# Performance work log

Measured on AMD Instinct MI355X. Metric: run time of the kernel, lower is better.

The kernel has to match this reference:

```python
import jax, jax.numpy as jnp
import numpy as np

B, N, NODE_DIM = 256, 200, 2
H, D, L, FF = 8, 128, 3, 512
KD = D // H  # key/val dim per head = 16
EPS = 1e-5


def _uniform(key, shape, fan):
    s = 1.0 / np.sqrt(fan)
    return jax.random.uniform(key, shape, jnp.float32, -s, s)


def setup_inputs() -> dict:
    key = jax.random.key(0)
    ks = jax.random.split(key, 16)
    return {
        "x": jax.random.normal(ks[0], (B, N, NODE_DIM), jnp.float32),
        "Wemb": _uniform(ks[1], (NODE_DIM, D), NODE_DIM),
        "bemb": _uniform(ks[2], (D,), NODE_DIM),
        "Wq": _uniform(ks[3], (L, H, D, KD), KD),
        "Wk": _uniform(ks[4], (L, H, D, KD), KD),
        "Wv": _uniform(ks[5], (L, H, D, KD), KD),
        "Wo": _uniform(ks[6], (L, H, KD, D), D),
        "bn1_g": jnp.ones((L, D), jnp.float32),
        "bn1_b": jnp.zeros((L, D), jnp.float32),
        "W1": _uniform(ks[7], (L, D, FF), D),
        "b1": _uniform(ks[8], (L, FF), D),
        "W2": _uniform(ks[9], (L, FF, D), FF),
        "b2": _uniform(ks[10], (L, D), FF),
        "bn2_g": jnp.ones((L, D), jnp.float32),
        "bn2_b": jnp.zeros((L, D), jnp.float32),
    }


def _batch_norm(h, g, b):
    # BatchNorm1d in training mode: stats over all (batch*graph) positions per channel
    hf = h.reshape(-1, h.shape[-1])
    m = hf.mean(axis=0)
    v = hf.var(axis=0)  # biased variance, as torch uses for normalization
    return (h - m) * jax.lax.rsqrt(v + EPS) * g + b


def _mha(h, Wq, Wk, Wv, Wo):
    # h: [B,N,D]; Wq/Wk/Wv: [H,D,KD]; Wo: [H,KD,D]
    Q = jnp.einsum('bnd,hdk->hbnk', h, Wq)
    K = jnp.einsum('bnd,hdk->hbnk', h, Wk)
    V = jnp.einsum('bnd,hdk->hbnk', h, Wv)
    scores = jnp.einsum('hbqk,hbnk->hbqn', Q, K) * (1.0 / np.sqrt(KD))
    attn = jax.nn.softmax(scores, axis=-1)
    heads = jnp.einsum('hbqn,hbnk->hbqk', attn, V)
    return jnp.einsum('hbqk,hkd->bqd', heads, Wo)


def reference(x, Wemb, bemb, Wq, Wk, Wv, Wo, bn1_g, bn1_b, W1, b1, W2, b2, bn2_g, bn2_b):
    h = x @ Wemb + bemb  # init_embed: [B,N,D]
    for l in range(L):
        h = h + _mha(h, Wq[l], Wk[l], Wv[l], Wo[l])
        h = _batch_norm(h, bn1_g[l], bn1_b[l])
        ff = jax.nn.relu(h @ W1[l] + b1[l]) @ W2[l] + b2[l]
        h = _batch_norm(h + ff, bn2_g[l], bn2_b[l])
    return (h, h.mean(axis=1))
```

## Files before the change

### kernel.cpp

```cpp
#include <hip/hip_runtime.h>
#include <math.h>

#define B_ 256
#define N_ 200
#define D_ 128
#define H_ 8
#define KD_ 16
#define L_ 3
#define FF_ 512
#define ROWS (B_*N_)
#define BND (ROWS*D_)

typedef float f32x4 __attribute__((ext_vector_type(4)));
typedef _Float16 f16x4 __attribute__((ext_vector_type(4)));
typedef _Float16 f16x8 __attribute__((ext_vector_type(8)));

__device__ __forceinline__ ushort f2h_bits(float f) {
  _Float16 h = (_Float16)f;
  union { _Float16 h; ushort u; } v; v.h = h; return v.u;
}
__device__ __forceinline__ void splith(float f, ushort& hi, ushort& lo) {
  _Float16 h = (_Float16)f;
  float hf = (float)h;
  _Float16 l = (_Float16)(f - hf);
  union { _Float16 h; ushort u; } a, b; a.h = h; b.h = l;
  hi = a.u; lo = b.u;
}

__global__ __launch_bounds__(256) void embed_kernel(const float* __restrict__ x,
    const float* __restrict__ Wemb, const float* __restrict__ bemb,
    float* __restrict__ hp, ushort* __restrict__ hhi, ushort* __restrict__ hlo)
{
  int i4 = blockIdx.x * 256 + threadIdx.x;
  int r  = i4 >> 5, c4 = i4 & 31;
  float x0 = x[2*r], x1 = x[2*r + 1];
  const float4 w0 = ((const float4*)Wemb)[c4];
  const float4 w1 = ((const float4*)Wemb)[32 + c4];
  const float4 bb = ((const float4*)bemb)[c4];
  float o[4];
  o[0] = fmaf(x0, w0.x, fmaf(x1, w1.x, bb.x));
  o[1] = fmaf(x0, w0.y, fmaf(x1, w1.y, bb.y));
  o[2] = fmaf(x0, w0.z, fmaf(x1, w1.z, bb.z));
  o[3] = fmaf(x0, w0.w, fmaf(x1, w1.w, bb.w));
  float4 of = { o[0], o[1], o[2], o[3] };
  ((float4*)hp)[i4] = of;
  ushort hi[4], lo[4];
#pragma unroll
  for (int k = 0; k < 4; k++) splith(o[k], hi[k], lo[k]);
  uint2 ph, pl;
  ph.x = (uint)hi[0] | ((uint)hi[1] << 16);
  ph.y = (uint)hi[2] | ((uint)hi[3] << 16);
  pl.x = (uint)lo[0] | ((uint)lo[1] << 16);
  pl.y = (uint)lo[2] | ((uint)lo[3] << 16);
  ((uint2*)hhi)[i4] = ph;
  ((uint2*)hlo)[i4] = pl;
}

__global__ __launch_bounds__(256) void t_wo(const float* __restrict__ Wo,
    ushort* __restrict__ dh)
{
  int i = blockIdx.x * 256 + threadIdx.x;
  int l = i / 16384, r = i % 16384;
  int n = r >> 7, k = r & 127;
  int hh = k >> 4, kd = k & 15;
  float w = Wo[l*16384 + hh*2048 + kd*128 + n];
  dh[i] = f2h_bits(w);
}
__global__ __launch_bounds__(256) void t_w2(const float* __restrict__ W2,
    ushort* __restrict__ dh)
{
  int i = blockIdx.x * 256 + threadIdx.x;
  int l = i / 65536, r = i % 65536;
  int d = r >> 9, f = r & 511;
  float w = W2[l*65536 + f*128 + d];
  dh[i] = f2h_bits(w);
}

__global__ __launch_bounds__(128) void init_scales(float* __restrict__ sc, float* __restrict__ sh)
{
  int c = threadIdx.x;
  sc[c] = 1.f;
  sh[c] = 0.f;
}

__global__ __launch_bounds__(128) void fold_qkv(const float* __restrict__ Wq,
    const float* __restrict__ Wk, const float* __restrict__ Wv,
    const float* __restrict__ sc, const float* __restrict__ sh,
    ushort* __restrict__ wh, float* __restrict__ bout)
{
  __shared__ float wsum[2];
  int n = blockIdx.x;
  int k = threadIdx.x;
  int which = n >> 7, hh = (n >> 4) & 7, kd = n & 15;
  const float* src = (which == 0) ? Wq : (which == 1) ? Wk : Wv;
  float w = src[hh*2048 + k*16 + kd];
  if (which == 0) w *= 0.25f * 1.44269504088896340736f;
  wh[n*128 + k] = f2h_bits(w * sc[k]);
  float p = sh[k] * w;
#pragma unroll
  for (int d = 1; d < 64; d <<= 1) p += __shfl_xor(p, d);
  if ((k & 63) == 0) wsum[k >> 6] = p;
  __syncthreads();
  if (k == 0) bout[n] = wsum[0] + wsum[1];
}

__global__ __launch_bounds__(128) void fold_w1(const float* __restrict__ W1,
    const float* __restrict__ b1, const float* __restrict__ sc, const float* __restrict__ sh,
    ushort* __restrict__ wh, float* __restrict__ bout)
{
  __shared__ float wsum[2];
  int f = blockIdx.x;
  int k = threadIdx.x;
  float w = W1[k*512 + f];
  wh[f*128 + k] = f2h_bits(w * sc[k]);
  float p = sh[k] * w;
#pragma unroll
  for (int d = 1; d < 64; d <<= 1) p += __shfl_xor(p, d);
  if ((k & 63) == 0) wsum[k >> 6] = p;
  __syncthreads();
  if (k == 0) bout[f] = b1[f] + wsum[0] + wsum[1];
}

template<int K, bool ALO, bool BIAS, bool RELU, bool RESIDBN,
         bool OUTQKV, bool OUT16, bool OUTHL, bool OUTF32, bool STATS>
__global__ __launch_bounds__(256, 2) void gemm_mfma(
    const ushort* __restrict__ Ahi, const ushort* __restrict__ Alo,
    const ushort* __restrict__ Wh,
    const float* __restrict__ bias,
    const float* __restrict__ residf, const float* __restrict__ rsc, const float* __restrict__ rsh,
    float* __restrict__ Cf, ushort* __restrict__ C16,
    ushort* __restrict__ Chl_hi, ushort* __restrict__ Chl_lo,
    float* __restrict__ psum, float* __restrict__ psq, int Ntot)
{
  __shared__ ushort AhiS[128*64];
  __shared__ ushort AloS[ALO ? 128*64 : 8];
  __shared__ ushort BhS [128*64];
  const int t    = threadIdx.x;
  const int bm   = blockIdx.y * 128;
  const int bn   = blockIdx.x * 128;
  const int lane = t & 63;
  const int w    = t >> 6, wm = w >> 1, wn = w & 1;
  const int quad = lane >> 4, l15 = lane & 15;

  f32x4 acc[4][4];
#pragma unroll
  for (int i = 0; i < 4; i++)
#pragma unroll
    for (int j = 0; j < 4; j++) acc[i][j] = (f32x4){0.f, 0.f, 0.f, 0.f};

  const ushort* AhiB = Ahi + (size_t)bm * K;
  const ushort* AloB = ALO ? (Alo + (size_t)bm * K) : nullptr;
  const ushort* BhB  = Wh  + (size_t)bn * K;

  for (int k0 = 0; k0 < K; k0 += 64) {
#pragma unroll
    for (int i = 0; i < 4; i++) {
      int idx = i * 256 + t;
      int row = idx >> 3, c = idx & 7;
      int k8  = c ^ (row & 7);
      size_t off = (size_t)row * K + k0 + k8 * 8;
      ((uint4*)AhiS)[idx] = *(const uint4*)(AhiB + off);
      if (ALO) ((uint4*)AloS)[idx] = *(const uint4*)(AloB + off);
      ((uint4*)BhS)[idx]  = *(const uint4*)(BhB + off);
    }
    __syncthreads();
#pragma unroll
    for (int ks = 0; ks < 2; ks++) {
      f16x8 ah[4], al[4], bh[4];
#pragma unroll
      for (int i = 0; i < 4; i++) {
        int row = wm * 64 + i * 16 + l15;
        int k8  = ks * 4 + quad;
        int ci  = k8 ^ (row & 7);
        ah[i] = ((const f16x8*)AhiS)[row * 8 + ci];
        if (ALO) al[i] = ((const f16x8*)AloS)[row * 8 + ci];
        int nrow = wn * 64 + i * 16 + l15;
        int cj   = k8 ^ (nrow & 7);
        bh[i] = ((const f16x8*)BhS)[nrow * 8 + cj];
      }
#pragma unroll
      for (int i = 0; i < 4; i++)
#pragma unroll
        for (int j = 0; j < 4; j++) {
          if (ALO) acc[i][j] = __builtin_amdgcn_mfma_f32_16x16x32_f16(al[i], bh[j], acc[i][j], 0, 0, 0);
          acc[i][j] = __builtin_amdgcn_mfma_f32_16x16x32_f16(ah[i], bh[j], acc[i][j], 0, 0, 0);
        }
    }
    __syncthreads();
  }

  float bv[4], scv[4], shv[4];
#pragma unroll
  for (int j = 0; j < 4; j++) {
    int col = bn + wn*64 + j*16 + l15;
    if (BIAS)    bv[j]  = bias[col];
    if (RESIDBN) { scv[j] = rsc[col]; shv[j] = rsh[col]; }
  }
  float sj[4] = {0.f,0.f,0.f,0.f}, qj[4] = {0.f,0.f,0.f,0.f};
#pragma unroll
  for (int i = 0; i < 4; i++) {
#pragma unroll
    for (int r = 0; r < 4; r++) {
      int row = bm + wm*64 + i*16 + quad*4 + r;
#pragma unroll
      for (int j = 0; j < 4; j++) {
        int col = bn + wn*64 + j*16 + l15;
        float v = acc[i][j][r];
        if (BIAS)    v += bv[j];
        if (RELU)    v = fmaxf(v, 0.f);
        if (RESIDBN) v += fmaf(residf[(size_t)row * Ntot + col], scv[j], shv[j]);
        if (OUTQKV) {
          if (bn < 256) {
            C16[(size_t)row * 256 + col] = f2h_bits(v);
          } else {
            ushort hi, lo; splith(v, hi, lo);
            Chl_hi[(size_t)row * 128 + (col - 256)] = hi;
            Chl_lo[(size_t)row * 128 + (col - 256)] = lo;
          }
        }
        if (OUT16) C16[(size_t)row * Ntot + col] = f2h_bits(v);
        if (OUTHL) {
          ushort hi, lo; splith(v, hi, lo);
          Chl_hi[(size_t)row * Ntot + col] = hi;
          Chl_lo[(size_t)row * Ntot + col] = lo;
        }
        if (OUTF32) Cf[(size_t)row * Ntot + col] = v;
        if (STATS) { sj[j] += v; qj[j] = fmaf(v, v, qj[j]); }
      }
    }
  }
  if (STATS) {
#pragma unroll
    for (int j = 0; j < 4; j++) {
      sj[j] += __shfl_xor(sj[j], 16); sj[j] += __shfl_xor(sj[j], 32);
      qj[j] += __shfl_xor(qj[j], 16); qj[j] += __shfl_xor(qj[j], 32);
    }
    float* ssum = (float*)AhiS;
    float* ssq  = ssum + 128;
    if (t < 128) { ssum[t] = 0.f; ssq[t] = 0.f; }
    __syncthreads();
    if (quad == 0) {
#pragma unroll
      for (int j = 0; j < 4; j++) {
        int col = wn*64 + j*16 + l15;
        atomicAdd(&ssum[col], sj[j]);
        atomicAdd(&ssq[col],  qj[j]);
      }
    }
    __syncthreads();
    if (t < 128) {
      psum[blockIdx.y * 128 + t] = ssum[t];
      psq [blockIdx.y * 128 + t] = ssq[t];
    }
  }
}

__global__ __launch_bounds__(256) void attn_kernel(const ushort* __restrict__ qk,
    const ushort* __restrict__ vh, const ushort* __restrict__ vl,
    ushort* __restrict__ hd)
{
  __shared__ __align__(16) _Float16 Ksh[208*24];
  __shared__ __align__(16) _Float16 VTh[16*216];
  __shared__ __align__(16) _Float16 VTl[16*216];
  const int b  = blockIdx.x >> 3;
  const int hh = blockIdx.x & 7;
  const int t  = threadIdx.x;
  const size_t rb = (size_t)b * N_;

  for (int i = t; i < 208*2; i += 256) {
    int n = i >> 1, half = i & 1;
    uint4 kv = {0u, 0u, 0u, 0u};
    if (n < N_) kv = *(const uint4*)(qk + (rb + n)*256 + 128 + hh*16 + half*8);
    *(uint4*)&Ksh[n*24 + half*8] = kv;
  }
  for (int i = t; i < 16*104; i += 256) {
    int kd = i & 15, n2 = i >> 4;
    int n0 = 2*n2, n1 = n0 + 1;
    ushort a0 = 0, a1 = 0, c0 = 0, c1 = 0;
    if (n0 < N_) { a0 = vh[(rb + n0)*128 + hh*16 + kd]; c0 = vl[(rb + n0)*128 + hh*16 + kd]; }
    if (n1 < N_) { a1 = vh[(rb + n1)*128 + hh*16 + kd]; c1 = vl[(rb + n1)*128 + hh*16 + kd]; }
    *(uint*)&VTh[kd*216 + n0] = (uint)a0 | ((uint)a1 << 16);
    *(uint*)&VTl[kd*216 + n0] = (uint)c0 | ((uint)c1 << 16);
  }
  __syncthreads();

  const int lane = t & 63;
  const int w    = t >> 6;
  const int l15  = lane & 15;
  const int g    = lane >> 4;

  for (int qt = w; qt < 13; qt += 4) {
    int qr  = qt*16 + l15;
    int qrc = qr < N_ ? qr : N_-1;
    f16x4 bq = *(const f16x4*)(qk + (rb + qrc)*256 + hh*16 + g*4);

    f32x4 ct[13];
#pragma unroll
    for (int kt = 0; kt < 13; kt++) {
      f16x4 ak = *(const f16x4*)&Ksh[(kt*16 + l15)*24 + g*4];
      ct[kt] = __builtin_amdgcn_mfma_f32_16x16x16f16(ak, bq, (f32x4){0.f,0.f,0.f,0.f}, 0, 0, 0);
    }
#pragma unroll
    for (int r = 0; r < 4; r++)
      if (g*4 + r >= 8) ct[12][r] = -1e30f;

    float m0 = -1e30f, m1 = -1e30f;
#pragma unroll
    for (int kt = 0; kt < 13; kt++) {
      m0 = fmaxf(m0, fmaxf(ct[kt][0], ct[kt][1]));
      m1 = fmaxf(m1, fmaxf(ct[kt][2], ct[kt][3]));
    }
    float m = fmaxf(m0, m1);
    m = fmaxf(m, __shfl_xor(m, 16));
    m = fmaxf(m, __shfl_xor(m, 32));

    float la0 = 0.f, la1 = 0.f, la2 = 0.f, la3 = 0.f;
#pragma unroll
    for (int kt = 0; kt < 13; kt++) {
      float p0 = __builtin_amdgcn_exp2f(ct[kt][0] - m);
      float p1 = __builtin_amdgcn_exp2f(ct[kt][1] - m);
      float p2 = __builtin_amdgcn_exp2f(ct[kt][2] - m);
      float p3 = __builtin_amdgcn_exp2f(ct[kt][3] - m);
      la0 += p0; la1 += p1; la2 += p2; la3 += p3;
      ct[kt][0] = p0; ct[kt][1] = p1; ct[kt][2] = p2; ct[kt][3] = p3;
    }
    float l = (la0 + la1) + (la2 + la3);
    l += __shfl_xor(l, 16);
    l += __shfl_xor(l, 32);

    f32x4 och = {0.f,0.f,0.f,0.f}, ocl = {0.f,0.f,0.f,0.f};
#pragma unroll
    for (int kt = 0; kt < 13; kt++) {
      f16x4 pt = { (_Float16)ct[kt][0], (_Float16)ct[kt][1],
                   (_Float16)ct[kt][2], (_Float16)ct[kt][3] };
      f16x4 avh = *(const f16x4*)&VTh[l15*216 + kt*16 + g*4];
      f16x4 avl = *(const f16x4*)&VTl[l15*216 + kt*16 + g*4];
      och = __builtin_amdgcn_mfma_f32_16x16x16f16(avh, pt, och, 0, 0, 0);
      ocl = __builtin_amdgcn_mfma_f32_16x16x16f16(avl, pt, ocl, 0, 0, 0);
    }

    if (qr < N_) {
      float inv = __builtin_amdgcn_rcpf(l);
      ushort o16[4];
#pragma unroll
      for (int r = 0; r < 4; r++) o16[r] = f2h_bits((och[r] + ocl[r]) * inv);
      uint2 p;
      p.x = (uint)o16[0] | ((uint)o16[1] << 16);
      p.y = (uint)o16[2] | ((uint)o16[3] << 16);
      *(uint2*)(hd + (rb + qr)*128 + hh*16 + g*4) = p;
    }
  }
}

__global__ __launch_bounds__(64) void bn_finalize(const float* __restrict__ psum,
    const float* __restrict__ psq, const float* __restrict__ g,
    const float* __restrict__ bta, float* __restrict__ scale, float* __restrict__ shift)
{
  int c = blockIdx.x;
  int i = threadIdx.x;
  float s = 0.f, q = 0.f;
  for (int r = i; r < 400; r += 64) { s += psum[r*128 + c]; q += psq[r*128 + c]; }
#pragma unroll
  for (int d = 32; d > 0; d >>= 1) { s += __shfl_down(s, d); q += __shfl_down(q, d); }
  if (i == 0) {
    const float invM = 1.f / 51200.f;
    float m  = s * invM;
    float v  = fmaf(q, invM, -m * m);
    float r  = rsqrtf(v + 1e-5f);
    float sc = r * g[c];
    scale[c] = sc;
    shift[c] = fmaf(-m, sc, bta[c]);
  }
}

__global__ __launch_bounds__(128) void bn_mean_final(float* __restrict__ hp,
    const float* __restrict__ scale, const float* __restrict__ shift,
    float* __restrict__ mout)
{
  int b = blockIdx.x, d = threadIdx.x;
  float sc = scale[d], sh = shift[d];
  float* p = hp + (size_t)b * N_ * D_ + d;
  float s = 0.f;
  for (int n = 0; n < N_; n++) {
    float v = fmaf(p[n * D_], sc, sh);
    p[n * D_] = v;
    s += v;
  }
  mout[b * D_ + d] = s * (1.f / N_);
}

extern "C" void kernel_launch(void* const* d_in, const int* in_sizes, int n_in,
                              void* d_out, int out_size, void* d_ws, size_t ws_size,
                              hipStream_t stream)
{
  const float* x    = (const float*)d_in[0];
  const float* Wemb = (const float*)d_in[1];
  const float* bemb = (const float*)d_in[2];
  const float* Wq   = (const float*)d_in[3];
  const float* Wk   = (const float*)d_in[4];
  const float* Wv   = (const float*)d_in[5];
  const float* Wo   = (const float*)d_in[6];
  const float* bn1g = (const float*)d_in[7];
  const float* bn1b = (const float*)d_in[8];
  const float* W1   = (const float*)d_in[9];
  const float* b1   = (const float*)d_in[10];
  const float* W2   = (const float*)d_in[11];
  const float* b2   = (const float*)d_in[12];
  const float* bn2g = (const float*)d_in[13];
  const float* bn2b = (const float*)d_in[14];
  float* out = (float*)d_out;

  float* hp = out;

  char* wsb = (char*)d_ws;
  ushort* h_hi  = (ushort*)wsb;
  ushort* h_lo  = (ushort*)(wsb + 13107200);
  char*   phase = wsb + 26214400;
  ushort* qkq   = (ushort*)phase;
  ushort* vhh   = (ushort*)(phase + 26214400);
  ushort* vll   = (ushort*)(phase + 39321600);
  ushort* hd    = (ushort*)(phase + 52428800);
  ushort* hid   = (ushort*)phase;
  char*   wp    = wsb + 91750400;
  ushort* woT   = (ushort*)wp;
  ushort* w2T   = (ushort*)(wp + 98304);
  ushort* fqkvw = (ushort*)(wp + 491520);
  ushort* fw1w  = (ushort*)(wp + 589824);
  float*  fqkv_b = (float*)(wp + 720896);
  float*  fw1_b  = (float*)(wp + 722432);
  float*  psum   = (float*)(wp + 724480);
  float*  psq    = (float*)(wp + 929280);
  float*  sc_a   = (float*)(wp + 1134080);
  float*  sh_a   = (float*)(wp + 1134592);
  float*  sc_b   = (float*)(wp + 1135104);
  float*  sh_b   = (float*)(wp + 1135616);

  embed_kernel<<<6400, 256, 0, stream>>>(x, Wemb, bemb, hp, h_hi, h_lo);
  t_wo<<<192, 256, 0, stream>>>(Wo, woT);
  t_w2<<<768, 256, 0, stream>>>(W2, w2T);
  init_scales<<<1, 128, 0, stream>>>(sc_b, sh_b);

  for (int l = 0; l < L_; l++) {
    fold_qkv<<<384, 128, 0, stream>>>(Wq + l*16384, Wk + l*16384, Wv + l*16384,
                                      sc_b, sh_b, fqkvw, fqkv_b);
    gemm_mfma<128, true, true, false, false, true, false, false, false, false>
        <<<dim3(3, 400), 256, 0, stream>>>(
        h_hi, h_lo, fqkvw, fqkv_b, nullptr, nullptr, nullptr,
        nullptr, qkq, vhh, vll, nullptr, nullptr, 384);
    attn_kernel<<<B_ * H_, 256, 0, stream>>>(qkq, vhh, vll, hd);
    gemm_mfma<128, false, false, false, true, false, false, true, true, true>
        <<<dim3(1, 400), 256, 0, stream>>>(
        hd, nullptr, woT + l*16384, nullptr, hp, sc_b, sh_b,
        hp, nullptr, h_hi, h_lo, psum, psq, 128);
    bn_finalize<<<128, 64, 0, stream>>>(psum, psq, bn1g + l*128, bn1b + l*128, sc_a, sh_a);
    fold_w1<<<512, 128, 0, stream>>>(W1 + l*65536, b1 + l*512, sc_a, sh_a, fw1w, fw1_b);
    gemm_mfma<128, true, true, true, false, false, true, false, false, false>
        <<<dim3(4, 400), 256, 0, stream>>>(
        h_hi, h_lo, fw1w, fw1_b, nullptr, nullptr, nullptr,
        nullptr, hid, nullptr, nullptr, nullptr, nullptr, 512);
    gemm_mfma<512, false, true, false, true, false, false, true, true, true>
        <<<dim3(1, 400), 256, 0, stream>>>(
        hid, nullptr, w2T + l*65536, b2 + l*128, hp, sc_a, sh_a,
        hp, nullptr, h_hi, h_lo, psum, psq, 128);
    bn_finalize<<<128, 64, 0, stream>>>(psum, psq, bn2g + l*128, bn2b + l*128, sc_b, sh_b);
  }

  bn_mean_final<<<B_, 128, 0, stream>>>(hp, sc_b, sh_b, out + BND);
}
```

Baseline: 624.3 us.

## Drop fp32 hidden state and store Q/K/V in head-major layout

Removes the fp32 copy of the hidden state; residual reads and the final output are reconstructed from the hi/lo fp16 split pair already maintained. Q, K and V are now written head-major so the attention kernel loads contiguous 16-element rows per head with vector loads, including V. This cuts global memory traffic in the residual GEMM epilogues and attention loads, at the cost of strided scalar stores in the QKV GEMM epilogue and hi+lo reconstruction precision for the residual.

```diff
diff --git a/kernel.cpp b/kernel.cpp
--- a/kernel.cpp
+++ b/kernel.cpp
@@ -19,6 +19,9 @@
   _Float16 h = (_Float16)f;
   union { _Float16 h; ushort u; } v; v.h = h; return v.u;
 }
+__device__ __forceinline__ float h2f(ushort u) {
+  union { ushort u; _Float16 h; } v; v.u = u; return (float)v.h;
+}
 __device__ __forceinline__ void splith(float f, ushort& hi, ushort& lo) {
   _Float16 h = (_Float16)f;
   float hf = (float)h;
@@ -29,7 +32,7 @@
 
 __global__ __launch_bounds__(256) void embed_kernel(const float* __restrict__ x,
     const float* __restrict__ Wemb, const float* __restrict__ bemb,
-    float* __restrict__ hp, ushort* __restrict__ hhi, ushort* __restrict__ hlo)
+    ushort* __restrict__ hhi, ushort* __restrict__ hlo)
 {
   int i4 = blockIdx.x * 256 + threadIdx.x;
   int r  = i4 >> 5, c4 = i4 & 31;
@@ -42,8 +45,6 @@
   o[1] = fmaf(x0, w0.y, fmaf(x1, w1.y, bb.y));
   o[2] = fmaf(x0, w0.z, fmaf(x1, w1.z, bb.z));
   o[3] = fmaf(x0, w0.w, fmaf(x1, w1.w, bb.w));
-  float4 of = { o[0], o[1], o[2], o[3] };
-  ((float4*)hp)[i4] = of;
   ushort hi[4], lo[4];
 #pragma unroll
   for (int k = 0; k < 4; k++) splith(o[k], hi[k], lo[k]);
@@ -122,14 +123,14 @@
 }
 
 template<int K, bool ALO, bool BIAS, bool RELU, bool RESIDBN,
-         bool OUTQKV, bool OUT16, bool OUTHL, bool OUTF32, bool STATS>
+         bool OUTQKV, bool OUT16, bool OUTHL, bool STATS>
 __global__ __launch_bounds__(256, 2) void gemm_mfma(
     const ushort* __restrict__ Ahi, const ushort* __restrict__ Alo,
     const ushort* __restrict__ Wh,
     const float* __restrict__ bias,
-    const float* __restrict__ residf, const float* __restrict__ rsc, const float* __restrict__ rsh,
-    float* __restrict__ Cf, ushort* __restrict__ C16,
-    ushort* __restrict__ Chl_hi, ushort* __restrict__ Chl_lo,
+    const ushort* rhi, const ushort* rlo,
+    const float* __restrict__ rsc, const float* __restrict__ rsh,
+    ushort* o0, ushort* o1, ushort* o2, ushort* o3,
     float* __restrict__ psum, float* __restrict__ psq, int Ntot)
 {
   __shared__ ushort AhiS[128*64];
@@ -208,23 +209,31 @@
         float v = acc[i][j][r];
         if (BIAS)    v += bv[j];
         if (RELU)    v = fmaxf(v, 0.f);
-        if (RESIDBN) v += fmaf(residf[(size_t)row * Ntot + col], scv[j], shv[j]);
+        if (RESIDBN) {
+          size_t ri = (size_t)row * Ntot + col;
+          float rr = h2f(rhi[ri]) + h2f(rlo[ri]);
+          v += fmaf(rr, scv[j], shv[j]);
+        }
         if (OUTQKV) {
-          if (bn < 256) {
-            C16[(size_t)row * 256 + col] = f2h_bits(v);
+          if (bn == 0) {
+            o0[((size_t)(col >> 4) * ROWS + row) * 16 + (col & 15)] = f2h_bits(v);
+          } else if (bn == 128) {
+            int c = col - 128;
+            o1[((size_t)(c >> 4) * ROWS + row) * 16 + (c & 15)] = f2h_bits(v);
           } else {
+            int c = col - 256;
             ushort hi, lo; splith(v, hi, lo);
-            Chl_hi[(size_t)row * 128 + (col - 256)] = hi;
-            Chl_lo[(size_t)row * 128 + (col - 256)] = lo;
+            size_t oi = ((size_t)(c >> 4) * ROWS + row) * 16 + (c & 15);
+            o2[oi] = hi;
+            o3[oi] = lo;
           }
         }
-        if (OUT16) C16[(size_t)row * Ntot + col] = f2h_bits(v);
+        if (OUT16) o0[(size_t)row * Ntot + col] = f2h_bits(v);
         if (OUTHL) {
           ushort hi, lo; splith(v, hi, lo);
-          Chl_hi[(size_t)row * Ntot + col] = hi;
-          Chl_lo[(size_t)row * Ntot + col] = lo;
+          o0[(size_t)row * Ntot + col] = hi;
+          o1[(size_t)row * Ntot + col] = lo;
         }
-        if (OUTF32) Cf[(size_t)row * Ntot + col] = v;
         if (STATS) { sj[j] += v; qj[j] = fmaf(v, v, qj[j]); }
       }
     }
@@ -255,9 +264,9 @@
   }
 }
 
-__global__ __launch_bounds__(256) void attn_kernel(const ushort* __restrict__ qk,
-    const ushort* __restrict__ vh, const ushort* __restrict__ vl,
-    ushort* __restrict__ hd)
+__global__ __launch_bounds__(256) void attn_kernel(const ushort* __restrict__ qs,
+    const ushort* __restrict__ ks, const ushort* __restrict__ vh,
+    const ushort* __restrict__ vl, ushort* __restrict__ hd)
 {
   __shared__ __align__(16) _Float16 Ksh[208*24];
   __shared__ __align__(16) _Float16 VTh[16*216];
@@ -266,21 +275,29 @@
   const int hh = blockIdx.x & 7;
   const int t  = threadIdx.x;
   const size_t rb = (size_t)b * N_;
+  const size_t hb = ((size_t)hh * ROWS + rb) * 16;
 
   for (int i = t; i < 208*2; i += 256) {
     int n = i >> 1, half = i & 1;
     uint4 kv = {0u, 0u, 0u, 0u};
-    if (n < N_) kv = *(const uint4*)(qk + (rb + n)*256 + 128 + hh*16 + half*8);
+    if (n < N_) kv = *(const uint4*)(ks + hb + n*16 + half*8);
     *(uint4*)&Ksh[n*24 + half*8] = kv;
   }
-  for (int i = t; i < 16*104; i += 256) {
-    int kd = i & 15, n2 = i >> 4;
-    int n0 = 2*n2, n1 = n0 + 1;
-    ushort a0 = 0, a1 = 0, c0 = 0, c1 = 0;
-    if (n0 < N_) { a0 = vh[(rb + n0)*128 + hh*16 + kd]; c0 = vl[(rb + n0)*128 + hh*16 + kd]; }
-    if (n1 < N_) { a1 = vh[(rb + n1)*128 + hh*16 + kd]; c1 = vl[(rb + n1)*128 + hh*16 + kd]; }
-    *(uint*)&VTh[kd*216 + n0] = (uint)a0 | ((uint)a1 << 16);
-    *(uint*)&VTl[kd*216 + n0] = (uint)c0 | ((uint)c1 << 16);
+  for (int i = t; i < 208*2; i += 256) {
+    int n = i >> 1, half = i & 1;
+    uint4 v0 = {0u, 0u, 0u, 0u};
+    if (n < N_) v0 = *(const uint4*)(vh + hb + n*16 + half*8);
+    const ushort* e = (const ushort*)&v0;
+#pragma unroll
+    for (int q = 0; q < 8; q++) ((ushort*)VTh)[(half*8 + q)*216 + n] = e[q];
+  }
+  for (int i = t; i < 208*2; i += 256) {
+    int n = i >> 1, half = i & 1;
+    uint4 v0 = {0u, 0u, 0u, 0u};
+    if (n < N_) v0 = *(const uint4*)(vl + hb + n*16 + half*8);
+    const ushort* e = (const ushort*)&v0;
+#pragma unroll
+    for (int q = 0; q < 8; q++) ((ushort*)VTl)[(half*8 + q)*216 + n] = e[q];
   }
   __syncthreads();
 
@@ -292,7 +309,7 @@
   for (int qt = w; qt < 13; qt += 4) {
     int qr  = qt*16 + l15;
     int qrc = qr < N_ ? qr : N_-1;
-    f16x4 bq = *(const f16x4*)(qk + (rb + qrc)*256 + hh*16 + g*4);
+    f16x4 bq = *(const f16x4*)(qs + hb + (size_t)qrc*16 + g*4);
 
     f32x4 ct[13];
 #pragma unroll
@@ -373,20 +390,21 @@
   }
 }
 
-__global__ __launch_bounds__(128) void bn_mean_final(float* __restrict__ hp,
+__global__ __launch_bounds__(128) void bn_mean_final(const ushort* __restrict__ hhi,
+    const ushort* __restrict__ hlo,
     const float* __restrict__ scale, const float* __restrict__ shift,
-    float* __restrict__ mout)
+    float* __restrict__ outh, float* __restrict__ mout)
 {
   int b = blockIdx.x, d = threadIdx.x;
   float sc = scale[d], sh = shift[d];
-  float* p = hp + (size_t)b * N_ * D_ + d;
   float s = 0.f;
   for (int n = 0; n < N_; n++) {
-    float v = fmaf(p[n * D_], sc, sh);
-    p[n * D_] = v;
+    size_t idx = ((size_t)b * N_ + n) * 128 + d;
+    float v = fmaf(h2f(hhi[idx]) + h2f(hlo[idx]), sc, sh);
+    outh[idx] = v;
     s += v;
   }
-  mout[b * D_ + d] = s * (1.f / N_);
+  mout[b * 128 + d] = s * (1.f / N_);
 }
 
 extern "C" void kernel_launch(void* const* d_in, const int* in_sizes, int n_in,
@@ -410,13 +428,12 @@
   const float* bn2b = (const float*)d_in[14];
   float* out = (float*)d_out;
 
-  float* hp = out;
-
   char* wsb = (char*)d_ws;
   ushort* h_hi  = (ushort*)wsb;
   ushort* h_lo  = (ushort*)(wsb + 13107200);
   char*   phase = wsb + 26214400;
-  ushort* qkq   = (ushort*)phase;
+  ushort* qsb   = (ushort*)phase;
+  ushort* ksb   = (ushort*)(phase + 13107200);
   ushort* vhh   = (ushort*)(phase + 26214400);
   ushort* vll   = (ushort*)(phase + 39321600);
   ushort* hd    = (ushort*)(phase + 52428800);
@@ -435,7 +452,7 @@
   float*  sc_b   = (float*)(wp + 1135104);
   float*  sh_b   = (float*)(wp + 1135616);
 
-  embed_kernel<<<6400, 256, 0, stream>>>(x, Wemb, bemb, hp, h_hi, h_lo);
+  embed_kernel<<<6400, 256, 0, stream>>>(x, Wemb, bemb, h_hi, h_lo);
   t_wo<<<192, 256, 0, stream>>>(Wo, woT);
   t_w2<<<768, 256, 0, stream>>>(W2, w2T);
   init_scales<<<1, 128, 0, stream>>>(sc_b, sh_b);
@@ -443,27 +460,27 @@
   for (int l = 0; l < L_; l++) {
     fold_qkv<<<384, 128, 0, stream>>>(Wq + l*16384, Wk + l*16384, Wv + l*16384,
                                       sc_b, sh_b, fqkvw, fqkv_b);
-    gemm_mfma<128, true, true, false, false, true, false, false, false, false>
+    gemm_mfma<128, true, true, false, false, true, false, false, false>
         <<<dim3(3, 400), 256, 0, stream>>>(
-        h_hi, h_lo, fqkvw, fqkv_b, nullptr, nullptr, nullptr,
-        nullptr, qkq, vhh, vll, nullptr, nullptr, 384);
-    attn_kernel<<<B_ * H_, 256, 0, stream>>>(qkq, vhh, vll, hd);
-    gemm_mfma<128, false, false, false, true, false, false, true, true, true>
+        h_hi, h_lo, fqkvw, fqkv_b, nullptr, nullptr, nullptr, nullptr,
+        qsb, ksb, vhh, vll, nullptr, nullptr, 384);
+    attn_kernel<<<B_ * H_, 256, 0, stream>>>(qsb, ksb, vhh, vll, hd);
+    gemm_mfma<128, false, false, false, true, false, false, true, true>
         <<<dim3(1, 400), 256, 0, stream>>>(
-        hd, nullptr, woT + l*16384, nullptr, hp, sc_b, sh_b,
-        hp, nullptr, h_hi, h_lo, psum, psq, 128);
+        hd, nullptr, woT + l*16384, nullptr, h_hi, h_lo, sc_b, sh_b,
+        h_hi, h_lo, nullptr, nullptr, psum, psq, 128);
     bn_finalize<<<128, 64, 0, stream>>>(psum, psq, bn1g + l*128, bn1b + l*128, sc_a, sh_a);
     fold_w1<<<512, 128, 0, stream>>>(W1 + l*65536, b1 + l*512, sc_a, sh_a, fw1w, fw1_b);
-    gemm_mfma<128, true, true, true, false, false, true, false, false, false>
+    gemm_mfma<128, true, true, true, false, false, true, false, false>
         <<<dim3(4, 400), 256, 0, stream>>>(
-        h_hi, h_lo, fw1w, fw1_b, nullptr, nullptr, nullptr,
-        nullptr, hid, nullptr, nullptr, nullptr, nullptr, 512);
-    gemm_mfma<512, false, true, false, true, false, false, true, true, true>
+        h_hi, h_lo, fw1w, fw1_b, nullptr, nullptr, nullptr, nullptr,
+        hid, nullptr, nullptr, nullptr, nullptr, nullptr, 512);
+    gemm_mfma<512, false, true, false, true, false, false, true, true>
         <<<dim3(1, 400), 256, 0, stream>>>(
-        hid, nullptr, w2T + l*65536, b2 + l*128, hp, sc_a, sh_a,
-        hp, nullptr, h_hi, h_lo, psum, psq, 128);
+        hid, nullptr, w2T + l*65536, b2 + l*128, h_hi, h_lo, sc_a, sh_a,
+        h_hi, h_lo, nullptr, nullptr, psum, psq, 128);
     bn_finalize<<<128, 64, 0, stream>>>(psum, psq, bn2g + l*128, bn2b + l*128, sc_b, sh_b);
   }
 
-  bn_mean_final<<<B_, 128, 0, stream>>>(hp, sc_b, sh_b, out + BND);
-}
+  bn_mean_final<<<B_, 128, 0, stream>>>(h_hi, h_lo, sc_b, sh_b, out, out + BND);
+}
```

Result: no change. 636.2 us (+1.9%).
